# Performance work log

Hardware: AMD Instinct MI355X
Metric: run time of the kernel (lower is better)

The kernel has to match this reference:

```python
import jax, jax.numpy as jnp
import numpy as np

# Dims: N batch, I input channels, C = in/hidden/attention/projection/out channels (all 128),
# streams=1, groups=1, spatial kernel 3, dropout 0.
N, I, C, H, W = 8, 128, 128, 36, 36


def _conv(x, w, pad):
    # x: [N, Cin, H, W], w: [Cout, Cin, kh, kw]
    return jax.lax.conv_general_dilated(
        x, w, (1, 1), pad, dimension_numbers=("NCHW", "OIHW", "NCHW"))


def _bias(b):
    return b[None, :, None, None]


def setup_inputs() -> dict:
    key = jax.random.key(0)
    ks = jax.random.split(key, 16)
    std = 0.05

    def w(k, o, i, s):
        return jax.random.normal(k, (o, i, s, s), jnp.float32) * std

    p = {}
    p["inp"] = jax.random.normal(ks[0], (N, I, H, W), jnp.float32)
    p["c0"] = jax.random.normal(ks[1], (1, C, 1, 1), jnp.float32)
    # proj_x: 1x1 conv input->in_channels, bias init 0
    p["w_x"] = w(ks[2], C, I, 1)
    p["b_x"] = jnp.zeros((C,), jnp.float32)
    # token convs (3x3, no bias); q uses SAME pad, k/v VALID
    p["w_qx"] = w(ks[3], C, C, 3)
    p["w_qc"] = w(ks[4], C, C, 3)
    scale = C ** (-0.5)  # gain = attn_channels^-0.5 on k projections
    p["w_kx"] = w(ks[5], C, C, 3) * scale
    p["w_kc"] = w(ks[6], C, C, 3) * scale
    p["w_vx"] = w(ks[7], C, C, 3)
    p["w_vc"] = w(ks[8], C, C, 3)
    # gating 1x1 convs: proj_z (bias=init_gate=1), proj_n (bias=0), in 2*proj channels
    p["w_z"] = w(ks[9], C, 2 * C, 1)
    p["b_z"] = jnp.ones((C,), jnp.float32)
    p["w_n"] = w(ks[10], C, 2 * C, 1)
    p["b_n"] = jnp.zeros((C,), jnp.float32)
    # proj_h: in_channels + 2*projection_channels -> hidden
    p["w_h"] = w(ks[11], C, 3 * C, 1)
    p["b_h"] = jnp.zeros((C,), jnp.float32)
    # output 1x1 conv hidden -> out_channels
    p["w_o"] = w(ks[12], C, C, 1)
    p["b_o"] = jnp.zeros((C,), jnp.float32)
    return p


def reference(inp, c0, w_x, b_x, w_qx, w_qc, w_kx, w_kc, w_vx, w_vc,
              w_z, b_z, w_n, b_n, w_h, b_h, w_o, b_o):
    # proj_x (1x1) -> x: [N, C, H, W]
    x = _conv(inp, w_x, "VALID") + _bias(b_x)
    n_, _, hh, ww = x.shape
    c = jnp.broadcast_to(c0, (n_, c0.shape[1], hh, ww))
    q_len = hh * ww
    # q: SAME pad -> Q = H*W tokens; k/v: VALID -> D = (H-2)*(W-2) tokens
    q = jnp.stack([_conv(x, w_qx, "SAME"), _conv(c, w_qc, "SAME")], 0)
    q = q.reshape(2, n_, -1, q_len)                      # [A, N, C, Q]
    k_x = _conv(x, w_kx, "VALID")
    d_len = k_x.shape[2] * k_x.shape[3]
    k = jnp.stack([k_x, _conv(c, w_kc, "VALID")], 0).reshape(2, n_, -1, d_len)   # [B, N, C, D]
    v = jnp.stack([_conv(x, w_vx, "VALID"), _conv(c, w_vc, "VALID")], 0)
    v = v.reshape(2, n_, -1, d_len)                      # [B, N, C, D]
    # all (A query source) x (B key/value source) attention pairs
    attn = jax.nn.softmax(jnp.einsum("ancq,bncd->anbqd", q, k), axis=-1)
    a = jnp.einsum("bncd,anbqd->anbcq", v, attn)         # [A, N, B, C, Q]
    a = a.reshape(2, n_, -1, hh, ww)                     # channels = B*C = 2*proj
    a_x, a_c = a[0], a[1]
    # GRU-style gated cell update (stored state; not part of the returned output)
    z = jax.nn.sigmoid(_conv(a_c, w_z, "VALID") + _bias(b_z))
    n_cand = jnp.tanh(_conv(a_c, w_n, "VALID") + _bias(b_n))
    c_new = z * c + (1.0 - z) * n_cand  # noqa: F841 (past['c'] in the original)
    # hidden: tanh(proj_h(cat[x, a_x])), dropout p=0 is identity
    xa = jnp.concatenate([x, a_x], axis=1)               # [N, 3*C, H, W]
    h = jnp.tanh(_conv(xa, w_h, "VALID") + _bias(b_h))
    return _conv(h, w_o, "VALID") + _bias(b_o)           # [N, C, H, W]
```

## Files before the change

kernel.cpp:

```cpp
#include <hip/hip_runtime.h>
#include <hip/hip_bf16.h>
#include <math.h>

#define NN 8
#define CH 128
#define HH 36
#define WWI 36
#define PP 1296
#define DD 1156
#define VP 1280
#define KC 1152
#define QT 81
#define DT 5

typedef __attribute__((ext_vector_type(8))) short short8;
typedef __attribute__((ext_vector_type(4))) float f32x4;

__device__ inline unsigned short f2bf(float f) {
    __hip_bfloat16 h = __float2bfloat16(f);
    return __builtin_bit_cast(unsigned short, h);
}
__device__ inline float fast_tanh(float x) {
    float e = __expf(2.f * x);
    return 1.f - 2.f / (e + 1.f);
}
#define MFMA(a, b, c) __builtin_amdgcn_mfma_f32_16x16x32_bf16((a), (b), (c), 0, 0, 0)

__global__ void k_setup(const float* __restrict__ wq, const float* __restrict__ wk,
                        const float* __restrict__ wv, const float* __restrict__ wh,
                        const float* __restrict__ wo, const float* __restrict__ wx,
                        const float* __restrict__ c0, const float* __restrict__ w_vc,
                        const float* __restrict__ b_h,
                        unsigned short* __restrict__ wcat, unsigned short* __restrict__ whb,
                        unsigned short* __restrict__ wob, unsigned short* __restrict__ wxb,
                        float* __restrict__ hconst)
{
    if (blockIdx.x == 576) {
        __shared__ float c0s[CH];
        __shared__ float part[256];
        __shared__ float vcs[CH];
        const int t = threadIdx.x;
        const int c = t & 127, half = t >> 7;
        if (t < CH) c0s[t] = c0[t];
        __syncthreads();
        {
            const float* row = w_vc + (size_t)c * 1152 + half * 576;
            float s = 0.f;
#pragma unroll 4
            for (int j4 = 0; j4 < 144; ++j4) {
                float4 v = ((const float4*)row)[j4];
                int j = half * 576 + j4 * 4;
                s += v.x * c0s[j / 9] + v.y * c0s[(j + 1) / 9]
                   + v.z * c0s[(j + 2) / 9] + v.w * c0s[(j + 3) / 9];
            }
            part[t] = s;
        }
        __syncthreads();
        if (t < CH) vcs[t] = part[t] + part[t + 128];
        __syncthreads();
        {
            const float* wrow = wh + (size_t)c * 384 + 256 + half * 64;
            float hs = 0.f;
#pragma unroll
            for (int j4 = 0; j4 < 16; ++j4) {
                float4 v = ((const float4*)wrow)[j4];
                int ci = half * 64 + j4 * 4;
                hs += v.x * vcs[ci] + v.y * vcs[ci + 1] + v.z * vcs[ci + 2] + v.w * vcs[ci + 3];
            }
            part[t] = hs;
        }
        __syncthreads();
        if (t < CH) hconst[t] = b_h[t] + part[t] + part[t + 128];
        return;
    }
    int t = blockIdx.x * 256 + threadIdx.x;
    int co = t / KC;
    int rem = t - co * KC;
    int tap = rem >> 7, ci = rem & 127;
    int iidx = co * KC + ci * 9 + tap;
    wcat[t] = f2bf(wq[iidx]);
    wcat[147456 + t] = f2bf(wk[iidx]);
    wcat[294912 + t] = f2bf(wv[iidx]);
    if (t < 32768) {
        int c2 = t >> 8, k2 = t & 255;
        whb[t] = f2bf(wh[c2 * 384 + k2]);
    }
    if (t < 16384) { wob[t] = f2bf(wo[t]); wxb[t] = f2bf(wx[t]); }
}

__global__ __launch_bounds__(64)
void k_proj(const float* __restrict__ inp, const unsigned short* __restrict__ wxb,
            const float* __restrict__ bx, unsigned short* __restrict__ xt)
{
    const int lane = threadIdx.x;
    const int quad = lane >> 4, lrow = lane & 15;
    const int p0 = blockIdx.x * 16;
    const int co0 = blockIdx.y * 64;
    const int n = blockIdx.z;
    const float* in_n = inp + (size_t)n * CH * PP;
    f32x4 acc[4] = {};

#pragma unroll
    for (int ks = 0; ks < 4; ++ks) {
        union { short8 v; unsigned short u[8]; } a;
        int ci0 = ks * 32 + quad * 8;
#pragma unroll
        for (int j = 0; j < 8; ++j)
            a.u[j] = f2bf(in_n[(size_t)(ci0 + j) * PP + p0 + lrow]);
#pragma unroll
        for (int ni = 0; ni < 4; ++ni) {
            short8 b = *(const short8*)&wxb[(size_t)(co0 + ni * 16 + lrow) * CH + ks * 32 + quad * 8];
            acc[ni] = MFMA(a.v, b, acc[ni]);
        }
    }
    unsigned short* xn = xt + (size_t)n * PP * CH;
#pragma unroll
    for (int ni = 0; ni < 4; ++ni) {
        float bv = bx[co0 + ni * 16 + lrow];
#pragma unroll
        for (int r = 0; r < 4; ++r)
            xn[(size_t)(p0 + quad * 4 + r) * CH + co0 + ni * 16 + lrow] = f2bf(acc[ni][r] + bv);
    }
}

__global__ __launch_bounds__(256)
void k_conv(const unsigned short* __restrict__ xt, const unsigned short* __restrict__ wcat,
            unsigned short* __restrict__ qt, unsigned short* __restrict__ kt,
            unsigned short* __restrict__ vb)
{
    __shared__ unsigned short lA[2][64 * 40];
    __shared__ unsigned short lB[2][128 * 40];
    const int t = threadIdx.x;
    const int wave = t >> 6, lane = t & 63;
    const int quad = lane >> 4, lrow = lane & 15;
    const int mode = blockIdx.y;
    const int n = blockIdx.z;
    const int limit = (mode == 0) ? PP : DD;
    const int tile0 = blockIdx.x * 64;
    if (tile0 >= limit) return;
    const unsigned short* xn = xt + (size_t)n * PP * CH;
    const unsigned short* wb = wcat + (size_t)mode * 128 * KC;

    const int arow = t >> 2, aseg = t & 3;
    int apr, apc;
    {
        int tok = tile0 + arow; if (tok >= limit) tok = limit - 1;
        int dv = (mode == 0) ? 36 : 34;
        apr = tok / dv; apc = tok - apr * dv;
    }

    uint4 ra, rb0, rb1;
    auto loadChunk = [&](int ks) {
        int tap = ks >> 2;
        int ky = tap / 3, kx = tap - ky * 3;
        int ci = (ks & 3) * 32 + aseg * 8;
        if (mode == 0) {
            int yy = apr + ky - 1, xx = apc + kx - 1;
            bool ok = (yy >= 0) && (yy < HH) && (xx >= 0) && (xx < WWI);
            ra = make_uint4(0, 0, 0, 0);
            if (ok) ra = *(const uint4*)&xn[(size_t)(yy * WWI + xx) * CH + ci];
        } else {
            int yy = apr + ky, xx = apc + kx;
            ra = *(const uint4*)&xn[(size_t)(yy * WWI + xx) * CH + ci];
        }
        rb0 = *(const uint4*)&wb[(size_t)arow * KC + ks * 32 + aseg * 8];
        rb1 = *(const uint4*)&wb[(size_t)(arow + 64) * KC + ks * 32 + aseg * 8];
    };
    auto storeChunk = [&](int buf) {
        *(uint4*)&lA[buf][arow * 40 + aseg * 8] = ra;
        *(uint4*)&lB[buf][arow * 40 + aseg * 8] = rb0;
        *(uint4*)&lB[buf][(arow + 64) * 40 + aseg * 8] = rb1;
    };

    f32x4 acc[4][2] = {};
    loadChunk(0);
    storeChunk(0);
    __syncthreads();

#pragma unroll
    for (int ks = 0; ks < 36; ++ks) {
        const int buf = ks & 1;
        if (ks < 35) loadChunk(ks + 1);
        short8 b0 = *(const short8*)&lB[buf][((wave * 2) * 16 + lrow) * 40 + quad * 8];
        short8 b1 = *(const short8*)&lB[buf][((wave * 2 + 1) * 16 + lrow) * 40 + quad * 8];
#pragma unroll
        for (int mi = 0; mi < 4; ++mi) {
            short8 a = *(const short8*)&lA[buf][(mi * 16 + lrow) * 40 + quad * 8];
            acc[mi][0] = MFMA(a, b0, acc[mi][0]);
            acc[mi][1] = MFMA(a, b1, acc[mi][1]);
        }
        if (ks < 35) storeChunk(buf ^ 1);
        __syncthreads();
    }

    if (mode == 0) {
        unsigned short* qn = qt + (size_t)n * PP * CH;
#pragma unroll
        for (int mi = 0; mi < 4; ++mi)
#pragma unroll
            for (int r = 0; r < 4; ++r) {
                int p = tile0 + mi * 16 + quad * 4 + r;
                if (p < PP)
#pragma unroll
                    for (int ni = 0; ni < 2; ++ni)
                        qn[(size_t)p * CH + (wave * 2 + ni) * 16 + lrow] = f2bf(acc[mi][ni][r]);
            }
    } else if (mode == 1) {
        unsigned short* kn = kt + (size_t)n * DD * CH;
#pragma unroll
        for (int mi = 0; mi < 4; ++mi)
#pragma unroll
            for (int r = 0; r < 4; ++r) {
                int d = tile0 + mi * 16 + quad * 4 + r;
                if (d < DD)
#pragma unroll
                    for (int ni = 0; ni < 2; ++ni)
                        kn[(size_t)d * CH + (wave * 2 + ni) * 16 + lrow] = f2bf(acc[mi][ni][r]);
            }
    } else {
        unsigned short* vn = vb + (size_t)n * CH * VP;
#pragma unroll
        for (int mi = 0; mi < 4; ++mi)
#pragma unroll
            for (int r = 0; r < 4; ++r) {
                int d = tile0 + mi * 16 + quad * 4 + r;
                if (d < DD)
#pragma unroll
                    for (int ni = 0; ni < 2; ++ni)
                        vn[(size_t)((wave * 2 + ni) * 16 + lrow) * VP + d] = f2bf(acc[mi][ni][r]);
            }
    }
}

__global__ __launch_bounds__(256)
void k_attn(const unsigned short* __restrict__ qt, const unsigned short* __restrict__ kt,
            const unsigned short* __restrict__ vb, _Float16* __restrict__ po,
            float* __restrict__ pm, float* __restrict__ pl)
{
    __shared__ unsigned short lS[2][128 * 40];
    __shared__ unsigned short lp[4][16 * 136];
    const int t = threadIdx.x;
    const int wave = t >> 6, lane = t & 63;
    const int quad = lane >> 4, lrow = lane & 15;
    const int qg = blockIdx.x;
    const int dt = blockIdx.y;
    const int n = blockIdx.z;
    const int qti = qg * 4 + wave;
    const int d0 = dt * 256;
    const unsigned short* qn = qt + (size_t)n * PP * CH;
    const unsigned short* kn = kt + (size_t)n * DD * CH;
    const unsigned short* vn = vb + (size_t)n * CH * VP;

    const int arow = t >> 2, aseg8 = (t & 3) * 8;
    const int lo0 = arow * 40 + aseg8;
    const int lo1 = (arow + 64) * 40 + aseg8;

    short8 qa[4];
    {
        int qrow = qti * 16 + lrow; if (qrow >= PP) qrow = PP - 1;
#pragma unroll
        for (int ks = 0; ks < 4; ++ks)
            qa[ks] = *(const short8*)&qn[(size_t)qrow * CH + ks * 32 + quad * 8];
    }

    f32x4 o[8] = {};
    float mx[4] = {-1e30f, -1e30f, -1e30f, -1e30f};
    float rs[4] = {0.f, 0.f, 0.f, 0.f};

#pragma unroll
    for (int h = 0; h < 2; ++h) {
        const int dbase = d0 + h * 128;
        int kr0 = dbase + arow;      if (kr0 >= DD) kr0 = DD - 1;
        int kr1 = dbase + arow + 64; if (kr1 >= DD) kr1 = DD - 1;
        const unsigned short* kp0 = kn + (size_t)kr0 * CH + aseg8;
        const unsigned short* kp1 = kn + (size_t)kr1 * CH + aseg8;
        const unsigned short* vp0 = vn + (size_t)arow * VP + dbase + aseg8;
        const unsigned short* vp1 = vn + (size_t)(arow + 64) * VP + dbase + aseg8;

        f32x4 s[8] = {};
        uint4 r0 = *(const uint4*)kp0;
        uint4 r1 = *(const uint4*)kp1;
        *(uint4*)&lS[0][lo0] = r0;
        *(uint4*)&lS[0][lo1] = r1;
        __syncthreads();
#pragma unroll
        for (int ks = 0; ks < 4; ++ks) {
            const int buf = ks & 1;
            if (ks < 3) {
                r0 = *(const uint4*)(kp0 + (ks + 1) * 32);
                r1 = *(const uint4*)(kp1 + (ks + 1) * 32);
            }
#pragma unroll
            for (int ni = 0; ni < 8; ++ni) {
                short8 b = *(const short8*)&lS[buf][(ni * 16 + lrow) * 40 + quad * 8];
                s[ni] = MFMA(qa[ks], b, s[ni]);
            }
            if (ks < 3) {
                *(uint4*)&lS[buf ^ 1][lo0] = r0;
                *(uint4*)&lS[buf ^ 1][lo1] = r1;
            }
            __syncthreads();
        }

#pragma unroll
        for (int ni = 0; ni < 8; ++ni)
            if (dbase + ni * 16 + lrow >= DD)
#pragma unroll
                for (int r = 0; r < 4; ++r) s[ni][r] = -1e30f;

        float hm[4] = {-1e30f, -1e30f, -1e30f, -1e30f};
#pragma unroll
        for (int ni = 0; ni < 8; ++ni)
#pragma unroll
            for (int r = 0; r < 4; ++r) hm[r] = fmaxf(hm[r], s[ni][r]);
#pragma unroll
        for (int off = 1; off < 16; off <<= 1)
#pragma unroll
            for (int r = 0; r < 4; ++r) hm[r] = fmaxf(hm[r], __shfl_xor(hm[r], off, 64));

        float m[4], sc[4];
#pragma unroll
        for (int r = 0; r < 4; ++r) {
            m[r] = fmaxf(mx[r], hm[r]);
            sc[r] = __expf(mx[r] - m[r]);
        }

        float hs[4] = {0.f, 0.f, 0.f, 0.f};
#pragma unroll
        for (int ni = 0; ni < 8; ++ni)
#pragma unroll
            for (int r = 0; r < 4; ++r) {
                float e = __expf(s[ni][r] - m[r]);
                s[ni][r] = e;
                hs[r] += e;
            }
#pragma unroll
        for (int off = 1; off < 16; off <<= 1)
#pragma unroll
            for (int r = 0; r < 4; ++r) hs[r] += __shfl_xor(hs[r], off, 64);
#pragma unroll
        for (int r = 0; r < 4; ++r) {
            rs[r] = rs[r] * sc[r] + hs[r];
            mx[r] = m[r];
        }
#pragma unroll
        for (int ni = 0; ni < 8; ++ni)
#pragma unroll
            for (int r = 0; r < 4; ++r) o[ni][r] *= sc[r];

#pragma unroll
        for (int ni = 0; ni < 8; ++ni)
#pragma unroll
            for (int r = 0; r < 4; ++r)
                lp[wave][(quad * 4 + r) * 136 + ni * 16 + lrow] = f2bf(s[ni][r]);

        r0 = *(const uint4*)vp0;
        r1 = *(const uint4*)vp1;
        *(uint4*)&lS[0][lo0] = r0;
        *(uint4*)&lS[0][lo1] = r1;
        __syncthreads();
#pragma unroll
        for (int ks = 0; ks < 4; ++ks) {
            const int buf = ks & 1;
            if (ks < 3) {
                r0 = *(const uint4*)(vp0 + (ks + 1) * 32);
                r1 = *(const uint4*)(vp1 + (ks + 1) * 32);
            }
            short8 pa = *(const short8*)&lp[wave][lrow * 136 + ks * 32 + quad * 8];
#pragma unroll
            for (int ni = 0; ni < 8; ++ni) {
                short8 b = *(const short8*)&lS[buf][(ni * 16 + lrow) * 40 + quad * 8];
                o[ni] = MFMA(pa, b, o[ni]);
            }
            if (ks < 3) {
                *(uint4*)&lS[buf ^ 1][lo0] = r0;
                *(uint4*)&lS[buf ^ 1][lo1] = r1;
            }
            __syncthreads();
        }
    }

    if (qti < QT) {
        const int base = (n * QT + qti) * DT + dt;
        _Float16* pob = po + (size_t)base * 2048;
#pragma unroll
        for (int ni = 0; ni < 8; ++ni)
#pragma unroll
            for (int r = 0; r < 4; ++r)
                pob[(quad * 4 + r) * 128 + ni * 16 + lrow] = (_Float16)o[ni][r];
        if (lrow == 0)
#pragma unroll
            for (int r = 0; r < 4; ++r) {
                pm[base * 16 + quad * 4 + r] = mx[r];
                pl[base * 16 + quad * 4 + r] = rs[r];
            }
    }
}

__global__ __launch_bounds__(256)
void k_ahout(const _Float16* __restrict__ po, const float* __restrict__ pm,
             const float* __restrict__ pl, const unsigned short* __restrict__ xt,
             const unsigned short* __restrict__ whb, const float* __restrict__ hconst,
             const unsigned short* __restrict__ wob, const float* __restrict__ bo,
             float* __restrict__ out)
{
    __shared__ float sm[80], ssc[80], smg[16], sli[16];
    __shared__ unsigned short la0[16 * 136];
    __shared__ unsigned short lh[16 * 136];
    const int qti = blockIdx.x;
    const int n = blockIdx.y;
    const int base = (n * QT + qti) * DT;
    const int t = threadIdx.x;

    if (t < 80) sm[t] = pm[base * 16 + t];
    __syncthreads();
    if (t < 16) {
        float mg = -1e30f;
#pragma unroll
        for (int dt = 0; dt < DT; ++dt) mg = fmaxf(mg, sm[dt * 16 + t]);
        float ls = 0.f;
#pragma unroll
        for (int dt = 0; dt < DT; ++dt) ls += __expf(sm[dt * 16 + t] - mg) * pl[base * 16 + dt * 16 + t];
        smg[t] = mg; sli[t] = 1.f / ls;
    }
    __syncthreads();
    if (t < 80) ssc[t] = __expf(sm[t] - smg[t & 15]);
    __syncthreads();
#pragma unroll
    for (int k = 0; k < 8; ++k) {
        int idx = t + k * 256;
        int row = idx >> 7, c = idx & 127;
        float acc = 0.f;
#pragma unroll
        for (int dt = 0; dt < DT; ++dt)
            acc += ssc[dt * 16 + row] * (float)po[(size_t)(base + dt) * 2048 + idx];
        la0[row * 136 + c] = f2bf(acc * sli[row]);
    }
    __syncthreads();

    const int wave = t >> 6, lane = t & 63;
    const int quad = lane >> 4, lrow = lane & 15;
    const int p0 = qti * 16;
    const unsigned short* x0 = xt + (size_t)n * PP * CH;

    f32x4 acc1[2] = {};
#pragma unroll
    for (int ks = 0; ks < 8; ++ks) {
        int col = (ks & 3) * 32 + quad * 8;
        short8 a;
        if (ks < 4) a = *(const short8*)&x0[(size_t)(p0 + lrow) * CH + col];
        else        a = *(const short8*)&la0[lrow * 136 + col];
#pragma unroll
        for (int j = 0; j < 2; ++j) {
            int ni = wave * 2 + j;
            short8 b = *(const short8*)&whb[(size_t)(ni * 16 + lrow) * 256 + ks * 32 + quad * 8];
            acc1[j] = MFMA(a, b, acc1[j]);
        }
    }
#pragma unroll
    for (int j = 0; j < 2; ++j) {
        int ni = wave * 2 + j;
        float hc = hconst[ni * 16 + lrow];
#pragma unroll
        for (int r = 0; r < 4; ++r)
            lh[(quad * 4 + r) * 136 + ni * 16 + lrow] = f2bf(fast_tanh(acc1[j][r] + hc));
    }
    __syncthreads();

    f32x4 acc2[2] = {};
#pragma unroll
    for (int ks = 0; ks < 4; ++ks) {
        short8 a = *(const short8*)&lh[lrow * 136 + ks * 32 + quad * 8];
#pragma unroll
        for (int j = 0; j < 2; ++j) {
            int ni = wave * 2 + j;
            short8 b = *(const short8*)&wob[(size_t)(ni * 16 + lrow) * CH + ks * 32 + quad * 8];
            acc2[j] = MFMA(a, b, acc2[j]);
        }
    }
#pragma unroll
    for (int j = 0; j < 2; ++j) {
        int ni = wave * 2 + j;
        float bv = bo[ni * 16 + lrow];
#pragma unroll
        for (int r = 0; r < 4; ++r)
            out[((size_t)(n * CH + ni * 16 + lrow)) * PP + p0 + quad * 4 + r] = acc2[j][r] + bv;
    }
}

extern "C" void kernel_launch(void* const* d_in, const int* in_sizes, int n_in,
                              void* d_out, int out_size, void* d_ws, size_t ws_size,
                              hipStream_t stream)
{
    const float* inp  = (const float*)d_in[0];
    const float* c0   = (const float*)d_in[1];
    const float* w_x  = (const float*)d_in[2];
    const float* b_x  = (const float*)d_in[3];
    const float* w_qx = (const float*)d_in[4];
    const float* w_kx = (const float*)d_in[6];
    const float* w_vx = (const float*)d_in[8];
    const float* w_vc = (const float*)d_in[9];
    const float* w_h  = (const float*)d_in[14];
    const float* b_h  = (const float*)d_in[15];
    const float* w_o  = (const float*)d_in[16];
    const float* b_o  = (const float*)d_in[17];
    float* out = (float*)d_out;

    char* w = (char*)d_ws;
    unsigned short* xt   = (unsigned short*)(w);
    unsigned short* qt   = (unsigned short*)(w + 2654208);
    unsigned short* kt   = (unsigned short*)(w + 5308416);
    unsigned short* vb   = (unsigned short*)(w + 7675904);
    unsigned short* wcat = (unsigned short*)(w + 12951552);
    unsigned short* wxb  = (unsigned short*)(w + 13836288);
    unsigned short* whb  = (unsigned short*)(w + 13869056);
    unsigned short* wob  = (unsigned short*)(w + 13934592);
    float* hconst        = (float*)(w + 13967360);
    float* pm            = (float*)(w + 13967872);
    float* pl            = (float*)(w + 14382592);
    _Float16* po         = (_Float16*)(w + 14797312);

    hipLaunchKernelGGL(k_setup, dim3(577), dim3(256), 0, stream,
                       w_qx, w_kx, w_vx, w_h, w_o, w_x, c0, w_vc, b_h,
                       wcat, whb, wob, wxb, hconst);

    hipLaunchKernelGGL(k_proj, dim3(QT, 2, NN), dim3(64), 0, stream, inp, wxb, b_x, xt);

    hipLaunchKernelGGL(k_conv, dim3(21, 3, NN), dim3(256), 0, stream, xt, wcat, qt, kt, vb);

    hipLaunchKernelGGL(k_attn, dim3(21, DT, NN), dim3(256), 0, stream, qt, kt, vb, po, pm, pl);

    hipLaunchKernelGGL(k_ahout, dim3(QT, NN), dim3(256), 0, stream,
                       po, pm, pl, xt, whb, hconst, wob, b_o, out);
}
```

Baseline: 192.7 us.

## Load conv weights directly into registers and double the K chunk per stage

The token conv kernel no longer stages weights through shared memory. Each wave now reads its own weight rows from global memory straight into registers, double-buffered in registers. The K step per iteration doubles from 32 to 64 channels, which halves the number of barriers and LDS round trips. The cost is more registers and uncoalesced per-lane global weight reads that depend on L2 hits, since four waves read overlapping data.

```diff
diff --git a/kernel.cpp b/kernel.cpp
--- a/kernel.cpp
+++ b/kernel.cpp
@@ -128,8 +128,7 @@
             unsigned short* __restrict__ qt, unsigned short* __restrict__ kt,
             unsigned short* __restrict__ vb)
 {
-    __shared__ unsigned short lA[2][64 * 40];
-    __shared__ unsigned short lB[2][128 * 40];
+    __shared__ unsigned short lA[2][64 * 72];
     const int t = threadIdx.x;
     const int wave = t >> 6, lane = t & 63;
     const int quad = lane >> 4, lrow = lane & 15;
@@ -148,48 +147,71 @@
         int dv = (mode == 0) ? 36 : 34;
         apr = tok / dv; apc = tok - apr * dv;
     }
-
-    uint4 ra, rb0, rb1;
-    auto loadChunk = [&](int ks) {
-        int tap = ks >> 2;
+    const unsigned short* wr0 = wb + (size_t)((wave * 2 + 0) * 16 + lrow) * KC;
+    const unsigned short* wr1 = wb + (size_t)((wave * 2 + 1) * 16 + lrow) * KC;
+
+    uint4 ra0, ra1;
+    auto loadA = [&](int ks) {
+        int tap = ks >> 1;
         int ky = tap / 3, kx = tap - ky * 3;
-        int ci = (ks & 3) * 32 + aseg * 8;
+        int ci = (ks & 1) * 64 + aseg * 16;
         if (mode == 0) {
             int yy = apr + ky - 1, xx = apc + kx - 1;
             bool ok = (yy >= 0) && (yy < HH) && (xx >= 0) && (xx < WWI);
-            ra = make_uint4(0, 0, 0, 0);
-            if (ok) ra = *(const uint4*)&xn[(size_t)(yy * WWI + xx) * CH + ci];
+            ra0 = make_uint4(0, 0, 0, 0);
+            ra1 = make_uint4(0, 0, 0, 0);
+            if (ok) {
+                const unsigned short* p = &xn[(size_t)(yy * WWI + xx) * CH + ci];
+                ra0 = *(const uint4*)p;
+                ra1 = *(const uint4*)(p + 8);
+            }
         } else {
             int yy = apr + ky, xx = apc + kx;
-            ra = *(const uint4*)&xn[(size_t)(yy * WWI + xx) * CH + ci];
-        }
-        rb0 = *(const uint4*)&wb[(size_t)arow * KC + ks * 32 + aseg * 8];
-        rb1 = *(const uint4*)&wb[(size_t)(arow + 64) * KC + ks * 32 + aseg * 8];
+            const unsigned short* p = &xn[(size_t)(yy * WWI + xx) * CH + ci];
+            ra0 = *(const uint4*)p;
+            ra1 = *(const uint4*)(p + 8);
+        }
     };
-    auto storeChunk = [&](int buf) {
-        *(uint4*)&lA[buf][arow * 40 + aseg * 8] = ra;
-        *(uint4*)&lB[buf][arow * 40 + aseg * 8] = rb0;
-        *(uint4*)&lB[buf][(arow + 64) * 40 + aseg * 8] = rb1;
+    auto storeA = [&](int buf) {
+        *(uint4*)&lA[buf][arow * 72 + aseg * 16] = ra0;
+        *(uint4*)&lA[buf][arow * 72 + aseg * 16 + 8] = ra1;
     };
 
+    short8 b0[2], b1[2], n0[2], n1[2];
+    auto loadB = [&](int ks, short8* d0, short8* d1) {
+        int off = (ks >> 1) * 128 + (ks & 1) * 64 + quad * 8;
+        d0[0] = *(const short8*)(wr0 + off);
+        d0[1] = *(const short8*)(wr0 + off + 32);
+        d1[0] = *(const short8*)(wr1 + off);
+        d1[1] = *(const short8*)(wr1 + off + 32);
+    };
+
     f32x4 acc[4][2] = {};
-    loadChunk(0);
-    storeChunk(0);
+    loadA(0);
+    storeA(0);
+    loadB(0, b0, b1);
     __syncthreads();
 
 #pragma unroll
-    for (int ks = 0; ks < 36; ++ks) {
+    for (int ks = 0; ks < 18; ++ks) {
         const int buf = ks & 1;
-        if (ks < 35) loadChunk(ks + 1);
-        short8 b0 = *(const short8*)&lB[buf][((wave * 2) * 16 + lrow) * 40 + quad * 8];
-        short8 b1 = *(const short8*)&lB[buf][((wave * 2 + 1) * 16 + lrow) * 40 + quad * 8];
-#pragma unroll
-        for (int mi = 0; mi < 4; ++mi) {
-            short8 a = *(const short8*)&lA[buf][(mi * 16 + lrow) * 40 + quad * 8];
-            acc[mi][0] = MFMA(a, b0, acc[mi][0]);
-            acc[mi][1] = MFMA(a, b1, acc[mi][1]);
-        }
-        if (ks < 35) storeChunk(buf ^ 1);
+        if (ks < 17) {
+            loadA(ks + 1);
+            loadB(ks + 1, n0, n1);
+        }
+#pragma unroll
+        for (int sub = 0; sub < 2; ++sub)
+#pragma unroll
+            for (int mi = 0; mi < 4; ++mi) {
+                short8 a = *(const short8*)&lA[buf][(mi * 16 + lrow) * 72 + sub * 32 + quad * 8];
+                acc[mi][0] = MFMA(a, b0[sub], acc[mi][0]);
+                acc[mi][1] = MFMA(a, b1[sub], acc[mi][1]);
+            }
+        if (ks < 17) {
+            storeA(buf ^ 1);
+            b0[0] = n0[0]; b0[1] = n0[1];
+            b1[0] = n1[0]; b1[1] = n1[1];
+        }
         __syncthreads();
     }
 
```

After: 193.7 us. Within noise of the previous version (+0.5%).
